# Kernel optimization log

Measured on AMD Instinct MI355X. Metric: run time of the kernel, lower is better.

## Reference

```python
import jax, jax.numpy as jnp
import numpy as np

N_HIDDEN_LAYERS = 9  # 32->32 middle layers (plus input 1->32 and output 32->1)
HID = 32
SLOPE = 0.01  # LeakyReLU negative_slope


def leaky_relu(x):
    return jnp.where(x >= 0, x, SLOPE * x)


def setup_inputs() -> dict:
    key = jax.random.key(0)
    ks = jax.random.split(key, 8)
    N = 1048576
    x = jax.random.normal(ks[0], (N,), dtype=jnp.float32)
    # PyTorch Linear init: U(-1/sqrt(fan_in), 1/sqrt(fan_in))
    def u(k, shape, fan_in):
        b = 1.0 / np.sqrt(fan_in)
        return jax.random.uniform(k, shape, jnp.float32, -b, b)
    W_in = u(ks[1], (1, HID), 1)
    b_in = u(ks[2], (HID,), 1)
    W_hid = u(ks[3], (N_HIDDEN_LAYERS, HID, HID), HID)
    b_hid = u(ks[4], (N_HIDDEN_LAYERS, HID), HID)
    W_out = u(ks[5], (HID, 1), HID)
    b_out = u(ks[6], (1,), HID)
    return {"x": x, "W_in": W_in, "b_in": b_in, "W_hid": W_hid,
            "b_hid": b_hid, "W_out": W_out, "b_out": b_out}


def reference(x, W_in, b_in, W_hid, b_hid, W_out, b_out):
    N = x.shape[0]
    h = x[:, None]  # [N, 1], mirrors x.reshape(N, 1)
    h = leaky_relu(h @ W_in + b_in)  # [N, 32]
    def step(h, wb):
        W, b = wb
        return leaky_relu(h @ W + b), None
    h, _ = jax.lax.scan(step, h, (W_hid, b_hid))
    out = h @ W_out + b_out  # [N, 1]
    return out.reshape(1, N)
```

## Files before the change

### kernel.cpp

```cpp
#include <hip/hip_runtime.h>

#define NLAYERS 9
#define HID 32
#define SLOPE 0.01f
#define NCHAIN 4

typedef _Float16 v2h __attribute__((ext_vector_type(2)));
typedef _Float16 v8h __attribute__((ext_vector_type(8)));
typedef float v4f __attribute__((ext_vector_type(4)));

union U8 { v8h v; v2h p[4]; };

__device__ __forceinline__ v2h pk_cvt(float a, float b) {
    return __builtin_bit_cast(v2h, __builtin_amdgcn_cvt_pkrtz(a, b));
}
__device__ __forceinline__ v2h leaky2(v2h t, v2h s) {
    return __builtin_elementwise_max(t, t * s);
}

__global__ __launch_bounds__(256, 2) void mlp_mfma_kernel(
    const float* __restrict__ x,
    const float* __restrict__ W_in,
    const float* __restrict__ b_in,
    const float* __restrict__ W_hid,
    const float* __restrict__ b_hid,
    const float* __restrict__ W_out,
    const float* __restrict__ b_out,
    float* __restrict__ out, int N)
{
    __shared__ __align__(16) _Float16 wfrag[NLAYERS][2][4][16][8];
    __shared__ __align__(16) v2h bias_sh[NLAYERS][4][4];

    for (int t = threadIdx.x; t < NLAYERS * HID * HID; t += blockDim.x) {
        int l = t >> 10;
        int rem = t & 1023;
        int k = rem >> 5, n = rem & 31;
        int a = (n >> 2) & 1;
        int g = k >> 3, j = k & 7;
        int c = ((n >> 3) << 2) | (n & 3);
        wfrag[l][a][g][c][j] = (_Float16)W_hid[t];
    }
    for (int t = threadIdx.x; t < NLAYERS * 16; t += blockDim.x) {
        int l = t >> 4, r = t & 15, g = r >> 2, j2 = r & 3;
        bias_sh[l][g][j2] = v2h{(_Float16)b_hid[l * HID + 8 * g + 2 * j2],
                                (_Float16)b_hid[l * HID + 8 * g + 2 * j2 + 1]};
    }
    __syncthreads();

    const int lane = threadIdx.x & 63;
    const int g    = lane >> 4;
    const int c    = lane & 15;

    v8h aW[NLAYERS][2];
#pragma unroll
    for (int l = 0; l < NLAYERS; ++l)
#pragma unroll
        for (int a = 0; a < 2; ++a)
            aW[l][a] = *(const v8h*)&wfrag[l][a][g][c][0];

    v2h win2[4], bin2[4], wout2[4];
#pragma unroll
    for (int u = 0; u < 4; ++u) {
        int d = 8 * g + 2 * u;
        win2[u]  = v2h{(_Float16)W_in[d],  (_Float16)W_in[d + 1]};
        bin2[u]  = v2h{(_Float16)b_in[d],  (_Float16)b_in[d + 1]};
        wout2[u] = v2h{(_Float16)W_out[d], (_Float16)W_out[d + 1]};
    }
    const float bo = b_out[0];
    const v2h slope2 = v2h{(_Float16)SLOPE, (_Float16)SLOPE};
    const v4f z4 = {};

    const int nwaves = (gridDim.x * blockDim.x) >> 6;
    const int wid    = (blockIdx.x * blockDim.x + threadIdx.x) >> 6;
    const int niter  = (N + NCHAIN * 16 - 1) / (NCHAIN * 16);

    float xc[NCHAIN];
#pragma unroll
    for (int ch = 0; ch < NCHAIN; ++ch) {
        int idx = wid * (NCHAIN * 16) + ch * 16 + c;
        xc[ch] = (wid < niter && idx < N) ? x[idx] : 0.0f;
    }

    for (int it = wid; it < niter; it += nwaves) {
        float xn[NCHAIN];
        {
            int nit = it + nwaves;
#pragma unroll
            for (int ch = 0; ch < NCHAIN; ++ch) {
                int idx = nit * (NCHAIN * 16) + ch * 16 + c;
                xn[ch] = (nit < niter && idx < N) ? x[idx] : 0.0f;
            }
        }

        U8 hb[NCHAIN];
#pragma unroll
        for (int ch = 0; ch < NCHAIN; ++ch) {
            _Float16 xh = (_Float16)xc[ch];
            v2h x2 = v2h{xh, xh};
#pragma unroll
            for (int u = 0; u < 4; ++u)
                hb[ch].p[u] = leaky2(x2 * win2[u] + bin2[u], slope2);
        }

#pragma unroll
        for (int l = 0; l < NLAYERS; ++l) {
            v2h bl0 = bias_sh[l][g][0], bl1 = bias_sh[l][g][1];
            v2h bl2 = bias_sh[l][g][2], bl3 = bias_sh[l][g][3];

            v4f a0[NCHAIN], a1[NCHAIN];
#pragma unroll
            for (int ch = 0; ch < NCHAIN; ++ch) {
                a0[ch] = __builtin_amdgcn_mfma_f32_16x16x32_f16(aW[l][0], hb[ch].v, z4, 0, 0, 0);
                a1[ch] = __builtin_amdgcn_mfma_f32_16x16x32_f16(aW[l][1], hb[ch].v, z4, 0, 0, 0);
            }
#pragma unroll
            for (int ch = 0; ch < NCHAIN; ++ch) {
                hb[ch].p[0] = leaky2(pk_cvt(a0[ch][0], a0[ch][1]) + bl0, slope2);
                hb[ch].p[1] = leaky2(pk_cvt(a0[ch][2], a0[ch][3]) + bl1, slope2);
                hb[ch].p[2] = leaky2(pk_cvt(a1[ch][0], a1[ch][1]) + bl2, slope2);
                hb[ch].p[3] = leaky2(pk_cvt(a1[ch][2], a1[ch][3]) + bl3, slope2);
            }
        }

#pragma unroll
        for (int ch = 0; ch < NCHAIN; ++ch) {
            float p = 0.0f;
#pragma unroll
            for (int u = 0; u < 4; ++u) {
                p = fmaf((float)hb[ch].p[u][0], (float)wout2[u][0], p);
                p = fmaf((float)hb[ch].p[u][1], (float)wout2[u][1], p);
            }
            p += __shfl_xor(p, 16, 64);
            p += __shfl_xor(p, 32, 64);
            float o = p + bo;
            int idx = it * (NCHAIN * 16) + ch * 16 + c;
            if (g == (ch & 3) && idx < N) out[idx] = o;
        }

#pragma unroll
        for (int ch = 0; ch < NCHAIN; ++ch) xc[ch] = xn[ch];
    }
}

extern "C" void kernel_launch(void* const* d_in, const int* in_sizes, int n_in,
                              void* d_out, int out_size, void* d_ws, size_t ws_size,
                              hipStream_t stream) {
    const float* x     = (const float*)d_in[0];
    const float* W_in  = (const float*)d_in[1];
    const float* b_in  = (const float*)d_in[2];
    const float* W_hid = (const float*)d_in[3];
    const float* b_hid = (const float*)d_in[4];
    const float* W_out = (const float*)d_in[5];
    const float* b_out = (const float*)d_in[6];
    float* out = (float*)d_out;

    int N = in_sizes[0];
    dim3 block(256);
    dim3 grid(1024);
    mlp_mfma_kernel<<<grid, block, 0, stream>>>(x, W_in, b_in, W_hid, b_hid,
                                                W_out, b_out, out, N);
}
```

Baseline: 105.3 us.

## Fold hidden bias into MFMA accumulator and widen per-wave chains to eight

Hidden-layer biases are stored as f32 in LDS and passed as the MFMA accumulator input, with the next layer's bias prefetched, removing the per-element packed bias add. The number of independent 16-row chains per wave doubles to raise MFMA ILP. The occupancy hint is dropped and the grid halved to match. Register pressure rises and occupancy may fall.

After: 122.4 us. 1.16x slower.

```diff
diff --git a/kernel.cpp b/kernel.cpp
--- a/kernel.cpp
+++ b/kernel.cpp
@@ -3,7 +3,7 @@
 #define NLAYERS 9
 #define HID 32
 #define SLOPE 0.01f
-#define NCHAIN 4
+#define NCHAIN 8
 
 typedef _Float16 v2h __attribute__((ext_vector_type(2)));
 typedef _Float16 v8h __attribute__((ext_vector_type(8)));
@@ -18,7 +18,7 @@
     return __builtin_elementwise_max(t, t * s);
 }
 
-__global__ __launch_bounds__(256, 2) void mlp_mfma_kernel(
+__global__ __launch_bounds__(256) void mlp_mfma_kernel(
     const float* __restrict__ x,
     const float* __restrict__ W_in,
     const float* __restrict__ b_in,
@@ -29,7 +29,7 @@
     float* __restrict__ out, int N)
 {
     __shared__ __align__(16) _Float16 wfrag[NLAYERS][2][4][16][8];
-    __shared__ __align__(16) v2h bias_sh[NLAYERS][4][4];
+    __shared__ __align__(16) float biasC[NLAYERS][2][4][4];
 
     for (int t = threadIdx.x; t < NLAYERS * HID * HID; t += blockDim.x) {
         int l = t >> 10;
@@ -40,10 +40,10 @@
         int c = ((n >> 3) << 2) | (n & 3);
         wfrag[l][a][g][c][j] = (_Float16)W_hid[t];
     }
-    for (int t = threadIdx.x; t < NLAYERS * 16; t += blockDim.x) {
-        int l = t >> 4, r = t & 15, g = r >> 2, j2 = r & 3;
-        bias_sh[l][g][j2] = v2h{(_Float16)b_hid[l * HID + 8 * g + 2 * j2],
-                                (_Float16)b_hid[l * HID + 8 * g + 2 * j2 + 1]};
+    for (int t = threadIdx.x; t < NLAYERS * HID; t += blockDim.x) {
+        int l = t >> 5, u = t & 31;
+        int g = u >> 3, a = (u >> 2) & 1, r = u & 3;
+        biasC[l][a][g][r] = b_hid[t];
     }
     __syncthreads();
 
@@ -57,6 +57,7 @@
 #pragma unroll
         for (int a = 0; a < 2; ++a)
             aW[l][a] = *(const v8h*)&wfrag[l][a][g][c][0];
+    asm volatile("" ::: "memory");
 
     v2h win2[4], bin2[4], wout2[4];
 #pragma unroll
@@ -68,7 +69,6 @@
     }
     const float bo = b_out[0];
     const v2h slope2 = v2h{(_Float16)SLOPE, (_Float16)SLOPE};
-    const v4f z4 = {};
 
     const int nwaves = (gridDim.x * blockDim.x) >> 6;
     const int wid    = (blockIdx.x * blockDim.x + threadIdx.x) >> 6;
@@ -102,24 +102,30 @@
                 hb[ch].p[u] = leaky2(x2 * win2[u] + bin2[u], slope2);
         }
 
+        v4f bc0 = *(const v4f*)&biasC[0][0][g][0];
+        v4f bc1 = *(const v4f*)&biasC[0][1][g][0];
 #pragma unroll
         for (int l = 0; l < NLAYERS; ++l) {
-            v2h bl0 = bias_sh[l][g][0], bl1 = bias_sh[l][g][1];
-            v2h bl2 = bias_sh[l][g][2], bl3 = bias_sh[l][g][3];
+            v4f nb0 = bc0, nb1 = bc1;
+            if (l + 1 < NLAYERS) {
+                nb0 = *(const v4f*)&biasC[l + 1][0][g][0];
+                nb1 = *(const v4f*)&biasC[l + 1][1][g][0];
+            }
 
             v4f a0[NCHAIN], a1[NCHAIN];
 #pragma unroll
             for (int ch = 0; ch < NCHAIN; ++ch) {
-                a0[ch] = __builtin_amdgcn_mfma_f32_16x16x32_f16(aW[l][0], hb[ch].v, z4, 0, 0, 0);
-                a1[ch] = __builtin_amdgcn_mfma_f32_16x16x32_f16(aW[l][1], hb[ch].v, z4, 0, 0, 0);
+                a0[ch] = __builtin_amdgcn_mfma_f32_16x16x32_f16(aW[l][0], hb[ch].v, bc0, 0, 0, 0);
+                a1[ch] = __builtin_amdgcn_mfma_f32_16x16x32_f16(aW[l][1], hb[ch].v, bc1, 0, 0, 0);
             }
 #pragma unroll
             for (int ch = 0; ch < NCHAIN; ++ch) {
-                hb[ch].p[0] = leaky2(pk_cvt(a0[ch][0], a0[ch][1]) + bl0, slope2);
-                hb[ch].p[1] = leaky2(pk_cvt(a0[ch][2], a0[ch][3]) + bl1, slope2);
-                hb[ch].p[2] = leaky2(pk_cvt(a1[ch][0], a1[ch][1]) + bl2, slope2);
-                hb[ch].p[3] = leaky2(pk_cvt(a1[ch][2], a1[ch][3]) + bl3, slope2);
+                hb[ch].p[0] = leaky2(pk_cvt(a0[ch][0], a0[ch][1]), slope2);
+                hb[ch].p[1] = leaky2(pk_cvt(a0[ch][2], a0[ch][3]), slope2);
+                hb[ch].p[2] = leaky2(pk_cvt(a1[ch][0], a1[ch][1]), slope2);
+                hb[ch].p[3] = leaky2(pk_cvt(a1[ch][2], a1[ch][3]), slope2);
             }
+            bc0 = nb0; bc1 = nb1;
         }
 
 #pragma unroll
@@ -156,7 +162,7 @@
 
     int N = in_sizes[0];
     dim3 block(256);
-    dim3 grid(1024);
+    dim3 grid(512);
     mlp_mfma_kernel<<<grid, block, 0, stream>>>(x, W_in, b_in, W_hid, b_hid,
                                                 W_out, b_out, out, N);
 }
```
